# Performance work log

Measured on AMD Instinct MI355X. Metric: run time of the kernel, lower is better.

## Reference

```python
import jax, jax.numpy as jnp
import numpy as np
import math

B, N, G, D = 32, 100, 32, 1024  # batch, boxes (hardcoded 100), groups/fc_dim, out_channel
DG = D // G                      # 32, per-group dim
FEAT_DIM = 64                    # position embedding dim


def setup_inputs() -> dict:
    key = jax.random.key(0)
    ks = jax.random.split(key, 10)
    feat = jax.random.normal(ks[0], (B, N, D), dtype=jnp.float32)
    # valid boxes: xmin/ymin in [0,500), width/height in [1,101)
    xy = jax.random.uniform(ks[1], (B, N, 2), dtype=jnp.float32) * 500.0
    wh = jax.random.uniform(ks[2], (B, N, 2), dtype=jnp.float32) * 100.0 + 1.0
    bbox = jnp.concatenate([xy, xy + wh], axis=-1)  # (B,N,4) xmin,ymin,xmax,ymax
    feat_mask = jax.random.bernoulli(ks[3], 0.1, (B, N, G, N))
    s = 0.02
    fc1_w = jax.random.normal(ks[4], (G, FEAT_DIM), dtype=jnp.float32) * s
    fc1_b = jnp.zeros((G,), dtype=jnp.float32)
    q_w = jax.random.normal(ks[5], (D, D), dtype=jnp.float32) * s
    q_b = jnp.zeros((D,), dtype=jnp.float32)
    k_w = jax.random.normal(ks[6], (D, D), dtype=jnp.float32) * s
    k_b = jnp.zeros((D,), dtype=jnp.float32)
    # grouped 1x1 conv: torch weight (D_out=1024, D_in/groups=1024,1,1) -> (G, DG, D)
    conv_w = jax.random.normal(ks[7], (G, DG, D), dtype=jnp.float32) * s
    conv_b = jnp.zeros((D,), dtype=jnp.float32)
    return {"feat": feat, "bbox": bbox, "feat_mask": feat_mask,
            "fc1_w": fc1_w, "fc1_b": fc1_b, "q_w": q_w, "q_b": q_b,
            "k_w": k_w, "k_b": k_b, "conv_w": conv_w, "conv_b": conv_b}


def _position_embedding(bbox):
    xmin, ymin, xmax, ymax = jnp.split(bbox, 4, axis=2)  # each (B,N,1)
    bw = xmax - xmin + 1.0
    bh = ymax - ymin + 1.0
    cx = 0.5 * (xmin + xmax)
    cy = 0.5 * (ymin + ymax)
    dx = jnp.log(jnp.maximum(jnp.abs((cx - cx.swapaxes(1, 2)) / bw), 1e-3))
    dy = jnp.log(jnp.maximum(jnp.abs((cy - cy.swapaxes(1, 2)) / bh), 1e-3))
    dw = jnp.log(bw / bw.swapaxes(1, 2))
    dh = jnp.log(bh / bh.swapaxes(1, 2))
    pos = jnp.stack([dx, dy, dw, dh], axis=3)  # (B,N,N,4)
    feat_range = jnp.arange(FEAT_DIM // 8, dtype=jnp.float32)  # 8
    dim_mat = jnp.power(1000.0, (8.0 / FEAT_DIM) * feat_range)  # (8,)
    div = (100.0 * pos)[..., None] / dim_mat  # (B,N,N,4,8)
    emb = jnp.concatenate([jnp.sin(div), jnp.cos(div)], axis=4)  # (B,N,N,4,16)
    return emb.reshape(bbox.shape[0], N, N, FEAT_DIM)


def reference(feat, bbox, feat_mask, fc1_w, fc1_b, q_w, q_b, k_w, k_b, conv_w, conv_b):
    pos_emb = _position_embedding(bbox)  # (B,N,N,64)
    # fc1 + relu -> affinity weights; aff_weight[b,q,g,k]
    aff_weight = jax.nn.relu(jnp.einsum('bqkf,gf->bqkg', pos_emb, fc1_w) + fc1_b)
    aff_weight = aff_weight.swapaxes(2, 3)  # (B,N,G,N)
    q = (feat @ q_w.T + q_b).reshape(-1, N, G, DG)  # (B,N,G,DG)
    k = (feat @ k_w.T + k_b).reshape(-1, N, G, DG)
    aff = jnp.einsum('bqgd,bkgd->bqgk', q, k) * (1.0 / math.sqrt(DG))  # (B,N,G,N)
    weighted = jnp.log(jnp.maximum(aff_weight, 1e-6)) + aff
    weighted = jnp.where(feat_mask, -1e9, weighted)
    sm = jax.nn.softmax(weighted, axis=3)  # (B,N,G,N)
    out_t = jnp.einsum('bqgk,bkc->bqgc', sm, feat)  # (B,N,G,D)
    # grouped 1x1 conv: group g maps D channels -> DG output channels
    lin = jnp.einsum('bqgc,goc->bqgo', out_t, conv_w) + conv_b.reshape(G, DG)
    attention = lin.reshape(feat.shape[0], N, D)
    return jax.nn.relu(feat + attention)
```

## Files before the change

### kernel.cpp

```cpp
#include <hip/hip_runtime.h>
#include <math.h>

#define B_  32
#define N_  100
#define G_  32
#define D_  1024
#define DG_ 32
#define FD_ 64

typedef __attribute__((ext_vector_type(8))) short short8;
typedef __attribute__((ext_vector_type(8))) unsigned short ushort8;
typedef __attribute__((ext_vector_type(4))) unsigned short ushort4v;
typedef __attribute__((ext_vector_type(4))) float f32x4;

__device__ inline unsigned short f2bf(float f) {
    unsigned int x = __float_as_uint(f);
    unsigned int r = (x + 0x7fffu + ((x >> 16) & 1u)) >> 16;
    return (unsigned short)r;
}
__device__ inline unsigned short f2h(float f) {
    _Float16 h = (_Float16)f;
    return __builtin_bit_cast(unsigned short, h);
}
__device__ inline float h2f(unsigned short u) {
    return (float)__builtin_bit_cast(_Float16, u);
}
__device__ inline void load_lds16(const void* g, void* l) {
    __builtin_amdgcn_global_load_lds(
        (const __attribute__((address_space(1))) void*)g,
        (__attribute__((address_space(3))) void*)l, 16, 0, 0);
}

__global__ __launch_bounds__(256) void prep_kernel(
    const unsigned int* __restrict__ mask, int* __restrict__ flag,
    const float* __restrict__ bbox, float* __restrict__ prep,
    const float* __restrict__ feat, unsigned short* __restrict__ featb,
    const float* __restrict__ qw, unsigned short* __restrict__ wqb,
    const float* __restrict__ kw, unsigned short* __restrict__ wkb,
    const float* __restrict__ cw, unsigned short* __restrict__ wcb)
{
    const int bid = blockIdx.x;
    const int t = threadIdx.x;
    if (bid < 256) {
        const int nwords = (B_ * N_ * G_ * N_) / 4 / 8;
        int v = 0;
        for (int i = bid * 256 + t; i < nwords; i += 256 * 256)
            v |= (mask[i] > 1u) ? 1 : 0;
        if (__any(v) && (t & 63) == 0) atomicOr(flag, 1);
        return;
    }
    if (bid < 272) {
        const int i = (bid - 256) * 256 + t;
        if (i < B_ * N_) {
            const float4 bb = *reinterpret_cast<const float4*>(bbox + (size_t)i * 4);
            const float bw = bb.z - bb.x + 1.0f, bh = bb.w - bb.y + 1.0f;
            float4 o0, o1;
            o0.x = 0.5f * (bb.x + bb.z);
            o0.y = 0.5f * (bb.y + bb.w);
            o0.z = __logf(bw);
            o0.w = __logf(bh);
            o1.x = 1.0f / bw;
            o1.y = 1.0f / bh;
            o1.z = 0.0f; o1.w = 0.0f;
            *reinterpret_cast<float4*>(prep + (size_t)i * 8)     = o0;
            *reinterpret_cast<float4*>(prep + (size_t)i * 8 + 4) = o1;
        }
        return;
    }
    const float* src;
    unsigned short* dst;
    int i;
    if (bid < 1872)      { src = feat; dst = featb; i = (bid - 272) * 256 + t; }
    else if (bid < 2384) { src = qw;   dst = wqb;   i = (bid - 1872) * 256 + t; }
    else if (bid < 2896) { src = kw;   dst = wkb;   i = (bid - 2384) * 256 + t; }
    else                 { src = cw;   dst = wcb;   i = (bid - 2896) * 256 + t; }
    const float4 a = reinterpret_cast<const float4*>(src)[i * 2 + 0];
    const float4 b = reinterpret_cast<const float4*>(src)[i * 2 + 1];
    ushort8 o;
    o[0] = f2bf(a.x); o[1] = f2bf(a.y); o[2] = f2bf(a.z); o[3] = f2bf(a.w);
    o[4] = f2bf(b.x); o[5] = f2bf(b.y); o[6] = f2bf(b.z); o[7] = f2bf(b.w);
    *reinterpret_cast<ushort8*>(&dst[i * 8]) = o;
}

__global__ __launch_bounds__(256) void mfma_gemm_nt(
    const unsigned short* __restrict__ A,
    const unsigned short* __restrict__ Wq,
    const unsigned short* __restrict__ Wk,
    const unsigned short* __restrict__ Wc,
    const float* __restrict__ bq, const float* __restrict__ bk,
    unsigned short* __restrict__ Q16, unsigned short* __restrict__ K16,
    unsigned short* __restrict__ F16)
{
    __shared__ short As0[128 * 64], As1[128 * 64];
    __shared__ short Bs0[64 * 64],  Bs1[64 * 64];

    const int z = blockIdx.z;
    const unsigned short* W = (z == 0) ? Wq : (z == 1) ? Wk : Wc;
    const float* bias        = (z == 0) ? bq : (z == 1) ? bk : nullptr;
    unsigned short* O        = (z == 0) ? Q16 : (z == 1) ? K16 : F16;

    const int m0 = blockIdx.x * 128;
    const int n0 = blockIdx.y * 64;
    const int t = threadIdx.x;
    const int lane = t & 63;
    const int wid = t >> 6;
    const int wr = wid >> 1, wc = wid & 1;
    const int lo = lane & 15, hi = lane >> 4;

    f32x4 acc[4][2] = {};

    auto STAGE = [&](short* dA, short* dB, int k0) {
#pragma unroll
        for (int c = 0; c < 4; ++c) {
            const int idx16 = c * 256 + t;
            const int row = idx16 >> 3;
            const int colb = ((idx16 & 7) * 16) ^ ((row & 7) << 4);
            load_lds16((const char*)(A + (size_t)(m0 + row) * D_ + k0) + colb,
                       (char*)dA + (c * 256 + wid * 64) * 16);
        }
#pragma unroll
        for (int c = 0; c < 2; ++c) {
            const int idx16 = c * 256 + t;
            const int row = idx16 >> 3;
            const int colb = ((idx16 & 7) * 16) ^ ((row & 7) << 4);
            load_lds16((const char*)(W + (size_t)(n0 + row) * D_ + k0) + colb,
                       (char*)dB + (c * 256 + wid * 64) * 16);
        }
    };

    auto COMPUTE = [&](const short* sA, const short* sB) {
#pragma unroll
        for (int ks = 0; ks < 2; ++ks) {
            short8 afr[4], bfr[2];
            const int kb = ks * 64 + hi * 16;
#pragma unroll
            for (int f = 0; f < 4; ++f) {
                const int am = wr * 64 + f * 16 + lo;
                afr[f] = *reinterpret_cast<const short8*>(
                    (const char*)sA + am * 128 + (kb ^ ((am & 7) << 4)));
            }
#pragma unroll
            for (int j = 0; j < 2; ++j) {
                const int bn = wc * 32 + j * 16 + lo;
                bfr[j] = *reinterpret_cast<const short8*>(
                    (const char*)sB + bn * 128 + (kb ^ ((bn & 7) << 4)));
            }
#pragma unroll
            for (int i = 0; i < 4; ++i)
#pragma unroll
                for (int j = 0; j < 2; ++j)
                    acc[i][j] = __builtin_amdgcn_mfma_f32_16x16x32_bf16(
                        afr[i], bfr[j], acc[i][j], 0, 0, 0);
        }
    };

    STAGE(As0, Bs0, 0);
    __syncthreads();
    for (int it = 0; it < 16; it += 2) {
        STAGE(As1, Bs1, (it + 1) << 6);
        COMPUTE(As0, Bs0);
        __syncthreads();
        if (it + 2 < 16) STAGE(As0, Bs0, (it + 2) << 6);
        COMPUTE(As1, Bs1);
        __syncthreads();
    }

#pragma unroll
    for (int j = 0; j < 2; ++j) {
        const int col = n0 + wc * 32 + j * 16 + lo;
        const float bv = bias ? bias[col] : 0.0f;
#pragma unroll
        for (int i = 0; i < 4; ++i) {
            const int mbase = m0 + wr * 64 + i * 16 + hi * 4;
#pragma unroll
            for (int r = 0; r < 4; ++r)
                O[(size_t)(mbase + r) * D_ + col] = f2bf(acc[i][j][r] + bv);
        }
    }
}

__global__ __launch_bounds__(256) void pos_fc1_kernel(
    const float* __restrict__ prep, const float* __restrict__ fc1_w,
    const float* __restrict__ fc1_b,
    const unsigned char* __restrict__ mask8, const int* __restrict__ mask32,
    const int* __restrict__ flag, unsigned short* __restrict__ wm)
{
    __shared__ unsigned short embh[112 * 72];
    __shared__ unsigned short w1h[G_ * 72];
    __shared__ float b1[G_];
    __shared__ float tbl[8];
    __shared__ float pos4[N_][4];

    const int b = blockIdx.x / N_;
    const int q = blockIdx.x % N_;
    const int t = threadIdx.x;
    const int lane = t & 63;
    const int w = t >> 6;
    const int lo = lane & 15, hi = lane >> 4;

    const float4 pq0 = *reinterpret_cast<const float4*>(prep + (size_t)(b * N_ + q) * 8);
    const float4 pq1 = *reinterpret_cast<const float4*>(prep + (size_t)(b * N_ + q) * 8 + 4);
    const float cxq = pq0.x, cyq = pq0.y, lbwq = pq0.z, lbhq = pq0.w;
    const float rbwq = pq1.x, rbhq = pq1.y;

    for (int i = t; i < G_ * FD_; i += 256)
        w1h[(i >> 6) * 72 + (i & 63)] = f2h(fc1_w[i]);
    if (t < G_) b1[t] = fc1_b[t];
    if (t < 8)  tbl[t] = 100.0f / powf(1000.0f, (float)t * 0.125f);
    for (int i = t; i < 12 * 64; i += 256)
        embh[(100 + (i >> 6)) * 72 + (i & 63)] = 0;

    if (t < N_) {
        const float4 p0 = *reinterpret_cast<const float4*>(prep + (size_t)(b * N_ + t) * 8);
        pos4[t][0] = __logf(fmaxf(fabsf(cxq - p0.x) * rbwq, 1e-3f));
        pos4[t][1] = __logf(fmaxf(fabsf(cyq - p0.y) * rbhq, 1e-3f));
        pos4[t][2] = lbwq - p0.z;
        pos4[t][3] = lbhq - p0.w;
    }
    __syncthreads();

    for (int idx = t; idx < N_ * 32; idx += 256) {
        const int k = idx >> 5;
        const int p = (idx >> 3) & 3;
        const int j = idx & 7;
        const float dv = pos4[k][p] * tbl[j];
        embh[k * 72 + p * 16 + j]     = f2h(__sinf(dv));
        embh[k * 72 + p * 16 + 8 + j] = f2h(__cosf(dv));
    }
    __syncthreads();

    const bool bytemask = (*flag != 0);
    const int xq = q & 7;
    for (int tid = w; tid < 14; tid += 4) {
        const int mt = tid >> 1, nt = tid & 1;
        f32x4 d = {};
#pragma unroll
        for (int ks = 0; ks < 2; ++ks) {
            const short8 af = *reinterpret_cast<const short8*>(
                embh + (mt * 16 + lo) * 72 + ks * 32 + hi * 8);
            const short8 bf = *reinterpret_cast<const short8*>(
                w1h + (nt * 16 + lo) * 72 + ks * 32 + hi * 8);
            d = __builtin_amdgcn_mfma_f32_16x16x32_f16(af, bf, d, 0, 0, 0);
        }
        const int g = nt * 16 + lo;
        const int k0 = mt * 16 + hi * 4;
        const float bb = b1[g];
        unsigned int mby = 0;
        uint4 mi = {};
        if (k0 < N_) {
            const size_t midx = ((size_t)(b * N_ + q) * G_ + g) * N_ + k0;
            if (bytemask) mby = *(const unsigned int*)(mask8 + midx);
            else          mi  = *(const uint4*)(mask32 + midx);
        }
        ushort4v ov;
#pragma unroll
        for (int r = 0; r < 4; ++r) {
            const int k = k0 + r;
            const bool msk = bytemask
                ? (((mby >> (8 * r)) & 0xffu) != 0u)
                : ((r == 0 ? mi.x : r == 1 ? mi.y : r == 2 ? mi.z : mi.w) != 0u);
            ov[r] = (k >= N_ || msk) ? (unsigned short)0
                                     : f2h(fmaxf(d[r] + bb, 1e-6f));
        }
        const size_t row = (size_t)(b * N_ + q) * G_ + g;
        char* dst = (char*)wm + row * 256 + ((2 * k0) ^ (xq << 4));
        *reinterpret_cast<ushort4v*>(dst) = ov;
    }
}

__global__ __launch_bounds__(256) void attn_mfma(
    const unsigned short* __restrict__ qb, const unsigned short* __restrict__ kb,
    const unsigned short* __restrict__ fk16, const unsigned short* __restrict__ wm,
    const float* __restrict__ feat, const float* __restrict__ conv_b,
    float* __restrict__ out)
{
    __shared__ unsigned short PW[128 * 128];
    __shared__ unsigned short FL[DG_ * 128];

    const int bg = blockIdx.x;
    const int b = bg >> 5, g = bg & 31;
    const int t = threadIdx.x;
    const int lane = t & 63;
    const int w = t >> 6;
    const int lo = lane & 15, hi = lane >> 4;
    const float scale = 0.17677669529663687f;

    {
        const char* wbase = (const char*)wm + ((size_t)b * N_ * G_ + g) * 256;
        for (int u = t; u < 1600; u += 256) {
            const int qq = u >> 4, seg = u & 15;
            load_lds16(wbase + (size_t)qq * (G_ * 256) + seg * 16,
                       (char*)PW + u * 16);
        }
    }
    for (int u = t; u < DG_ * 28; u += 256) {
        const int dg = u / 28, n = 100 + u % 28;
        *(unsigned short*)((char*)FL + dg * 256 +
                           (((n >> 3) ^ (dg & 7)) << 4) + (n & 7) * 2) = 0;
    }
    for (int u = t; u < 400; u += 256) {
        const int n = u >> 2, c4 = u & 3;
        const ushort8 v = *reinterpret_cast<const ushort8*>(
            fk16 + (size_t)(b * N_ + n) * D_ + g * DG_ + c4 * 8);
#pragma unroll
        for (int j = 0; j < 8; ++j) {
            const int dg = c4 * 8 + j;
            *(unsigned short*)((char*)FL + dg * 256 +
                               (((n >> 3) ^ j) << 4) + (n & 7) * 2) = v[j];
        }
    }

    short8 qf[2], kf[7];
#pragma unroll
    for (int mtl = 0; mtl < 2; ++mtl) {
        const int row = w * 32 + mtl * 16 + lo;
        const int rc = row < N_ ? row : N_ - 1;
        qf[mtl] = *reinterpret_cast<const short8*>(
            qb + (size_t)(b * N_ + rc) * D_ + g * DG_ + hi * 8);
    }
#pragma unroll
    for (int ct = 0; ct < 7; ++ct) {
        const int kr = ct * 16 + lo;
        const int krc = kr < N_ ? kr : N_ - 1;
        kf[ct] = *reinterpret_cast<const short8*>(
            kb + (size_t)(b * N_ + krc) * D_ + g * DG_ + hi * 8);
    }

    __syncthreads();

    f32x4 s[2][7];
#pragma unroll
    for (int mtl = 0; mtl < 2; ++mtl)
#pragma unroll
        for (int ct = 0; ct < 7; ++ct) {
            f32x4 z = {};
            s[mtl][ct] = __builtin_amdgcn_mfma_f32_16x16x32_bf16(
                qf[mtl], kf[ct], z, 0, 0, 0);
        }

    float sm[2][4];
#pragma unroll
    for (int mtl = 0; mtl < 2; ++mtl) {
        const int qr0 = w * 32 + mtl * 16 + hi * 4;
        f32x4 mv = s[mtl][0];
#pragma unroll
        for (int ct = 1; ct < 7; ++ct)
#pragma unroll
            for (int r = 0; r < 4; ++r) mv[r] = fmaxf(mv[r], s[mtl][ct][r]);
        float mx[4];
#pragma unroll
        for (int r = 0; r < 4; ++r) {
            float m = mv[r];
            m = fmaxf(m, __shfl_xor(m, 1));
            m = fmaxf(m, __shfl_xor(m, 2));
            m = fmaxf(m, __shfl_xor(m, 4));
            m = fmaxf(m, __shfl_xor(m, 8));
            mx[r] = m;
        }
        f32x4 sv = {};
#pragma unroll
        for (int ct = 0; ct < 7; ++ct) {
            const int k = ct * 16 + lo;
#pragma unroll
            for (int r = 0; r < 4; ++r) {
                const int row = qr0 + r;
                const float wv = h2f(*(const unsigned short*)(
                    (const char*)PW + row * 256 + ((2 * k) ^ ((row & 7) << 4))));
                const float e = __expf((s[mtl][ct][r] - mx[r]) * scale) * wv;
                s[mtl][ct][r] = e;
                sv[r] += e;
            }
        }
#pragma unroll
        for (int r = 0; r < 4; ++r) {
            float ss = sv[r];
            ss += __shfl_xor(ss, 1);
            ss += __shfl_xor(ss, 2);
            ss += __shfl_xor(ss, 4);
            ss += __shfl_xor(ss, 8);
            sm[mtl][r] = 1.0f / ss;
        }
    }

#pragma unroll
    for (int mtl = 0; mtl < 2; ++mtl) {
        const int qr0 = w * 32 + mtl * 16 + hi * 4;
#pragma unroll
        for (int ct = 0; ct < 7; ++ct) {
            const int col = ct * 16 + lo;
#pragma unroll
            for (int r = 0; r < 4; ++r) {
                const int row = qr0 + r;
                *(unsigned short*)((char*)PW + row * 256 +
                                   ((2 * col) ^ ((row & 7) << 4))) =
                    f2bf(s[mtl][ct][r] * sm[mtl][r]);
            }
        }
    }
    {
        const int zr = w * 32 + (lane & 31);
        const int zg = 14 + (lane >> 5);
        short8 zs = {};
        *reinterpret_cast<short8*>(
            (char*)PW + zr * 256 + ((zg * 16) ^ ((zr & 7) << 4))) = zs;
    }

    f32x4 o[2][2] = {};
#pragma unroll
    for (int ks = 0; ks < 4; ++ks) {
        short8 pa[2], fb[2];
#pragma unroll
        for (int mtl = 0; mtl < 2; ++mtl) {
            const int prow = w * 32 + mtl * 16 + lo;
            pa[mtl] = *reinterpret_cast<const short8*>(
                (const char*)PW + prow * 256 +
                ((ks * 64 + hi * 16) ^ ((prow & 7) << 4)));
        }
#pragma unroll
        for (int nt = 0; nt < 2; ++nt) {
            const int dg = nt * 16 + lo;
            fb[nt] = *reinterpret_cast<const short8*>(
                (const char*)FL + dg * 256 +
                ((ks * 64 + hi * 16) ^ ((dg & 7) << 4)));
        }
#pragma unroll
        for (int mtl = 0; mtl < 2; ++mtl)
#pragma unroll
            for (int nt = 0; nt < 2; ++nt)
                o[mtl][nt] = __builtin_amdgcn_mfma_f32_16x16x32_bf16(
                    pa[mtl], fb[nt], o[mtl][nt], 0, 0, 0);
    }

#pragma unroll
    for (int mtl = 0; mtl < 2; ++mtl) {
        const int qr0 = w * 32 + mtl * 16 + hi * 4;
#pragma unroll
        for (int nt = 0; nt < 2; ++nt) {
            const int col = g * DG_ + nt * 16 + lo;
            const float cb = conv_b[col];
#pragma unroll
            for (int r = 0; r < 4; ++r) {
                const int q = qr0 + r;
                if (q < N_) {
                    const size_t gi = (size_t)(b * N_ + q) * D_ + col;
                    out[gi] = fmaxf(feat[gi] + o[mtl][nt][r] + cb, 0.0f);
                }
            }
        }
    }
}

extern "C" void kernel_launch(void* const* d_in, const int* in_sizes, int n_in,
                              void* d_out, int out_size, void* d_ws, size_t ws_size,
                              hipStream_t stream)
{
    const float* feat   = (const float*)d_in[0];
    const float* bbox   = (const float*)d_in[1];
    const void*  maskp  = d_in[2];
    const float* fc1_w  = (const float*)d_in[3];
    const float* fc1_b  = (const float*)d_in[4];
    const float* q_w    = (const float*)d_in[5];
    const float* q_b    = (const float*)d_in[6];
    const float* k_w    = (const float*)d_in[7];
    const float* k_b    = (const float*)d_in[8];
    const float* conv_w = (const float*)d_in[9];
    const float* conv_b = (const float*)d_in[10];

    const int BN_D  = B_ * N_ * D_;
    const int DD    = D_ * D_;
    const int WM_N  = B_ * G_ * N_ * 128;

    unsigned short* ws16 = (unsigned short*)d_ws;
    unsigned short* qb16  = ws16;
    unsigned short* kb16  = qb16 + BN_D;
    unsigned short* fk16  = kb16 + BN_D;
    unsigned short* wm    = fk16 + BN_D;
    int* flag = (int*)(wm + WM_N);
    float* prep = (float*)(flag + 64);

    unsigned short* featb = wm;
    unsigned short* wqb   = featb + BN_D;
    unsigned short* wkb   = wqb + DD;
    unsigned short* wcb   = wkb + DD;

    hipMemsetAsync(flag, 0, sizeof(int), stream);
    prep_kernel<<<3408, 256, 0, stream>>>((const unsigned int*)maskp, flag,
                                          bbox, prep, feat, featb,
                                          q_w, wqb, k_w, wkb, conv_w, wcb);

    dim3 gg(B_ * N_ / 128, D_ / 64, 3);
    mfma_gemm_nt<<<gg, 256, 0, stream>>>(featb, wqb, wkb, wcb, q_b, k_b,
                                         qb16, kb16, fk16);

    pos_fc1_kernel<<<B_ * N_, 256, 0, stream>>>(prep, fc1_w, fc1_b,
                                                (const unsigned char*)maskp,
                                                (const int*)maskp, flag, wm);

    attn_mfma<<<B_ * G_, 256, 0, stream>>>(qb16, kb16, fk16, wm,
                                           feat, conv_b, (float*)d_out);
}
```

Baseline: 96.82 us.

## Fuse cast and position-fc1 kernels, split mask detection, read bf16 residual

The bf16 cast work and the position-embedding/fc1 work now share one launch, with even and odd blocks interleaved. The bbox preprocessing moves into each block's shared memory and mask detection becomes its own small kernel. featb no longer aliases wm and gets its own workspace region, so the epilogue reads the bf16 feature copy instead of fp32 for the residual. This is meant to cut launch overhead and overlap the two independent workloads, but the residual add now loses precision and the workspace footprint grows.

```diff
diff --git a/kernel.cpp b/kernel.cpp
--- a/kernel.cpp
+++ b/kernel.cpp
@@ -25,61 +25,147 @@
 __device__ inline float h2f(unsigned short u) {
     return (float)__builtin_bit_cast(_Float16, u);
 }
+__device__ inline float bf2f(unsigned short u) {
+    return __uint_as_float((unsigned int)u << 16);
+}
 __device__ inline void load_lds16(const void* g, void* l) {
     __builtin_amdgcn_global_load_lds(
         (const __attribute__((address_space(1))) void*)g,
         (__attribute__((address_space(3))) void*)l, 16, 0, 0);
 }
 
-__global__ __launch_bounds__(256) void prep_kernel(
-    const unsigned int* __restrict__ mask, int* __restrict__ flag,
-    const float* __restrict__ bbox, float* __restrict__ prep,
+__global__ __launch_bounds__(256) void detect_kernel(
+    const unsigned int* __restrict__ m, int* __restrict__ flag)
+{
+    const int nwords = (B_ * N_ * G_ * N_) / 4 / 8;
+    int v = 0;
+    for (int i = blockIdx.x * 256 + threadIdx.x; i < nwords; i += 256 * 256)
+        v |= (m[i] > 1u) ? 1 : 0;
+    if (__any(v) && (threadIdx.x & 63) == 0) atomicOr(flag, 1);
+}
+
+__global__ __launch_bounds__(256) void fused_cast_pos(
+    const float* __restrict__ bbox, const float* __restrict__ fc1_w,
+    const float* __restrict__ fc1_b,
+    const unsigned char* __restrict__ mask8, const int* __restrict__ mask32,
+    const int* __restrict__ flag, unsigned short* __restrict__ wm,
     const float* __restrict__ feat, unsigned short* __restrict__ featb,
     const float* __restrict__ qw, unsigned short* __restrict__ wqb,
     const float* __restrict__ kw, unsigned short* __restrict__ wkb,
     const float* __restrict__ cw, unsigned short* __restrict__ wcb)
 {
+    __shared__ unsigned short embh[112 * 72];
+    __shared__ unsigned short w1h[G_ * 72];
+    __shared__ float b1[G_];
+    __shared__ float tbl[8];
+    __shared__ float pos4[N_][4];
+    __shared__ float prepL[N_][6];
+
     const int bid = blockIdx.x;
     const int t = threadIdx.x;
-    if (bid < 256) {
-        const int nwords = (B_ * N_ * G_ * N_) / 4 / 8;
-        int v = 0;
-        for (int i = bid * 256 + t; i < nwords; i += 256 * 256)
-            v |= (mask[i] > 1u) ? 1 : 0;
-        if (__any(v) && (t & 63) == 0) atomicOr(flag, 1);
+
+    if ((bid & 1) == 0) {
+        const int pid = bid >> 1;
+        const float* src;
+        unsigned short* dst;
+        int i;
+        if (pid < 1600)      { src = feat; dst = featb; i = pid * 256 + t; }
+        else if (pid < 2112) { src = qw;   dst = wqb;   i = (pid - 1600) * 256 + t; }
+        else if (pid < 2624) { src = kw;   dst = wkb;   i = (pid - 2112) * 256 + t; }
+        else if (pid < 3136) { src = cw;   dst = wcb;   i = (pid - 2624) * 256 + t; }
+        else return;
+        const float4 a = reinterpret_cast<const float4*>(src)[i * 2 + 0];
+        const float4 b = reinterpret_cast<const float4*>(src)[i * 2 + 1];
+        ushort8 o;
+        o[0] = f2bf(a.x); o[1] = f2bf(a.y); o[2] = f2bf(a.z); o[3] = f2bf(a.w);
+        o[4] = f2bf(b.x); o[5] = f2bf(b.y); o[6] = f2bf(b.z); o[7] = f2bf(b.w);
+        *reinterpret_cast<ushort8*>(&dst[i * 8]) = o;
         return;
     }
-    if (bid < 272) {
-        const int i = (bid - 256) * 256 + t;
-        if (i < B_ * N_) {
-            const float4 bb = *reinterpret_cast<const float4*>(bbox + (size_t)i * 4);
-            const float bw = bb.z - bb.x + 1.0f, bh = bb.w - bb.y + 1.0f;
-            float4 o0, o1;
-            o0.x = 0.5f * (bb.x + bb.z);
-            o0.y = 0.5f * (bb.y + bb.w);
-            o0.z = __logf(bw);
-            o0.w = __logf(bh);
-            o1.x = 1.0f / bw;
-            o1.y = 1.0f / bh;
-            o1.z = 0.0f; o1.w = 0.0f;
-            *reinterpret_cast<float4*>(prep + (size_t)i * 8)     = o0;
-            *reinterpret_cast<float4*>(prep + (size_t)i * 8 + 4) = o1;
-        }
-        return;
-    }
-    const float* src;
-    unsigned short* dst;
-    int i;
-    if (bid < 1872)      { src = feat; dst = featb; i = (bid - 272) * 256 + t; }
-    else if (bid < 2384) { src = qw;   dst = wqb;   i = (bid - 1872) * 256 + t; }
-    else if (bid < 2896) { src = kw;   dst = wkb;   i = (bid - 2384) * 256 + t; }
-    else                 { src = cw;   dst = wcb;   i = (bid - 2896) * 256 + t; }
-    const float4 a = reinterpret_cast<const float4*>(src)[i * 2 + 0];
-    const float4 b = reinterpret_cast<const float4*>(src)[i * 2 + 1];
-    ushort8 o;
-    o[0] = f2bf(a.x); o[1] = f2bf(a.y); o[2] = f2bf(a.z); o[3] = f2bf(a.w);
-    o[4] = f2bf(b.x); o[5] = f2bf(b.y); o[6] = f2bf(b.z); o[7] = f2bf(b.w);
-    *reinterpret_cast<ushort8*>(&dst[i * 8]) = o;
+
+    const int pid = bid >> 1;
+    const int b = pid / N_;
+    const int q = pid % N_;
+    const int lane = t & 63;
+    const int w = t >> 6;
+    const int lo = lane & 15, hi = lane >> 4;
+
+    if (t < N_) {
+        const float4 bb = *reinterpret_cast<const float4*>(bbox + (size_t)(b * N_ + t) * 4);
+        const float bw = bb.z - bb.x + 1.0f, bh = bb.w - bb.y + 1.0f;
+        prepL[t][0] = 0.5f * (bb.x + bb.z);
+        prepL[t][1] = 0.5f * (bb.y + bb.w);
+        prepL[t][2] = __logf(bw);
+        prepL[t][3] = __logf(bh);
+        prepL[t][4] = 1.0f / bw;
+        prepL[t][5] = 1.0f / bh;
+    }
+    for (int i = t; i < G_ * FD_; i += 256)
+        w1h[(i >> 6) * 72 + (i & 63)] = f2h(fc1_w[i]);
+    if (t < G_) b1[t] = fc1_b[t];
+    if (t < 8)  tbl[t] = 100.0f / powf(1000.0f, (float)t * 0.125f);
+    for (int i = t; i < 12 * 64; i += 256)
+        embh[(100 + (i >> 6)) * 72 + (i & 63)] = 0;
+    __syncthreads();
+
+    const float cxq = prepL[q][0], cyq = prepL[q][1];
+    const float lbwq = prepL[q][2], lbhq = prepL[q][3];
+    const float rbwq = prepL[q][4], rbhq = prepL[q][5];
+    if (t < N_) {
+        pos4[t][0] = __logf(fmaxf(fabsf(cxq - prepL[t][0]) * rbwq, 1e-3f));
+        pos4[t][1] = __logf(fmaxf(fabsf(cyq - prepL[t][1]) * rbhq, 1e-3f));
+        pos4[t][2] = lbwq - prepL[t][2];
+        pos4[t][3] = lbhq - prepL[t][3];
+    }
+    __syncthreads();
+
+    for (int idx = t; idx < N_ * 32; idx += 256) {
+        const int k = idx >> 5;
+        const int p = (idx >> 3) & 3;
+        const int j = idx & 7;
+        const float dv = pos4[k][p] * tbl[j];
+        embh[k * 72 + p * 16 + j]     = f2h(__sinf(dv));
+        embh[k * 72 + p * 16 + 8 + j] = f2h(__cosf(dv));
+    }
+    __syncthreads();
+
+    const bool bytemask = (*flag != 0);
+    const int xq = q & 7;
+    for (int tid = w; tid < 14; tid += 4) {
+        const int mt = tid >> 1, nt = tid & 1;
+        f32x4 d = {};
+#pragma unroll
+        for (int ks = 0; ks < 2; ++ks) {
+            const short8 af = *reinterpret_cast<const short8*>(
+                embh + (mt * 16 + lo) * 72 + ks * 32 + hi * 8);
+            const short8 bf = *reinterpret_cast<const short8*>(
+                w1h + (nt * 16 + lo) * 72 + ks * 32 + hi * 8);
+            d = __builtin_amdgcn_mfma_f32_16x16x32_f16(af, bf, d, 0, 0, 0);
+        }
+        const int g = nt * 16 + lo;
+        const int k0 = mt * 16 + hi * 4;
+        const float bb = b1[g];
+        unsigned int mby = 0;
+        uint4 mi = {};
+        if (k0 < N_) {
+            const size_t midx = ((size_t)(b * N_ + q) * G_ + g) * N_ + k0;
+            if (bytemask) mby = *(const unsigned int*)(mask8 + midx);
+            else          mi  = *(const uint4*)(mask32 + midx);
+        }
+        ushort4v ov;
+#pragma unroll
+        for (int r = 0; r < 4; ++r) {
+            const int k = k0 + r;
+            const bool msk = bytemask
+                ? (((mby >> (8 * r)) & 0xffu) != 0u)
+                : ((r == 0 ? mi.x : r == 1 ? mi.y : r == 2 ? mi.z : mi.w) != 0u);
+            ov[r] = (k >= N_ || msk) ? (unsigned short)0
+                                     : f2h(fmaxf(d[r] + bb, 1e-6f));
+        }
+        const size_t row = (size_t)(b * N_ + q) * G_ + g;
+        char* dst = (char*)wm + row * 256 + ((2 * k0) ^ (xq << 4));
+        *reinterpret_cast<ushort4v*>(dst) = ov;
+    }
 }
 
 __global__ __launch_bounds__(256) void mfma_gemm_nt(
@@ -179,99 +265,10 @@
     }
 }
 
-__global__ __launch_bounds__(256) void pos_fc1_kernel(
-    const float* __restrict__ prep, const float* __restrict__ fc1_w,
-    const float* __restrict__ fc1_b,
-    const unsigned char* __restrict__ mask8, const int* __restrict__ mask32,
-    const int* __restrict__ flag, unsigned short* __restrict__ wm)
-{
-    __shared__ unsigned short embh[112 * 72];
-    __shared__ unsigned short w1h[G_ * 72];
-    __shared__ float b1[G_];
-    __shared__ float tbl[8];
-    __shared__ float pos4[N_][4];
-
-    const int b = blockIdx.x / N_;
-    const int q = blockIdx.x % N_;
-    const int t = threadIdx.x;
-    const int lane = t & 63;
-    const int w = t >> 6;
-    const int lo = lane & 15, hi = lane >> 4;
-
-    const float4 pq0 = *reinterpret_cast<const float4*>(prep + (size_t)(b * N_ + q) * 8);
-    const float4 pq1 = *reinterpret_cast<const float4*>(prep + (size_t)(b * N_ + q) * 8 + 4);
-    const float cxq = pq0.x, cyq = pq0.y, lbwq = pq0.z, lbhq = pq0.w;
-    const float rbwq = pq1.x, rbhq = pq1.y;
-
-    for (int i = t; i < G_ * FD_; i += 256)
-        w1h[(i >> 6) * 72 + (i & 63)] = f2h(fc1_w[i]);
-    if (t < G_) b1[t] = fc1_b[t];
-    if (t < 8)  tbl[t] = 100.0f / powf(1000.0f, (float)t * 0.125f);
-    for (int i = t; i < 12 * 64; i += 256)
-        embh[(100 + (i >> 6)) * 72 + (i & 63)] = 0;
-
-    if (t < N_) {
-        const float4 p0 = *reinterpret_cast<const float4*>(prep + (size_t)(b * N_ + t) * 8);
-        pos4[t][0] = __logf(fmaxf(fabsf(cxq - p0.x) * rbwq, 1e-3f));
-        pos4[t][1] = __logf(fmaxf(fabsf(cyq - p0.y) * rbhq, 1e-3f));
-        pos4[t][2] = lbwq - p0.z;
-        pos4[t][3] = lbhq - p0.w;
-    }
-    __syncthreads();
-
-    for (int idx = t; idx < N_ * 32; idx += 256) {
-        const int k = idx >> 5;
-        const int p = (idx >> 3) & 3;
-        const int j = idx & 7;
-        const float dv = pos4[k][p] * tbl[j];
-        embh[k * 72 + p * 16 + j]     = f2h(__sinf(dv));
-        embh[k * 72 + p * 16 + 8 + j] = f2h(__cosf(dv));
-    }
-    __syncthreads();
-
-    const bool bytemask = (*flag != 0);
-    const int xq = q & 7;
-    for (int tid = w; tid < 14; tid += 4) {
-        const int mt = tid >> 1, nt = tid & 1;
-        f32x4 d = {};
-#pragma unroll
-        for (int ks = 0; ks < 2; ++ks) {
-            const short8 af = *reinterpret_cast<const short8*>(
-                embh + (mt * 16 + lo) * 72 + ks * 32 + hi * 8);
-            const short8 bf = *reinterpret_cast<const short8*>(
-                w1h + (nt * 16 + lo) * 72 + ks * 32 + hi * 8);
-            d = __builtin_amdgcn_mfma_f32_16x16x32_f16(af, bf, d, 0, 0, 0);
-        }
-        const int g = nt * 16 + lo;
-        const int k0 = mt * 16 + hi * 4;
-        const float bb = b1[g];
-        unsigned int mby = 0;
-        uint4 mi = {};
-        if (k0 < N_) {
-            const size_t midx = ((size_t)(b * N_ + q) * G_ + g) * N_ + k0;
-            if (bytemask) mby = *(const unsigned int*)(mask8 + midx);
-            else          mi  = *(const uint4*)(mask32 + midx);
-        }
-        ushort4v ov;
-#pragma unroll
-        for (int r = 0; r < 4; ++r) {
-            const int k = k0 + r;
-            const bool msk = bytemask
-                ? (((mby >> (8 * r)) & 0xffu) != 0u)
-                : ((r == 0 ? mi.x : r == 1 ? mi.y : r == 2 ? mi.z : mi.w) != 0u);
-            ov[r] = (k >= N_ || msk) ? (unsigned short)0
-                                     : f2h(fmaxf(d[r] + bb, 1e-6f));
-        }
-        const size_t row = (size_t)(b * N_ + q) * G_ + g;
-        char* dst = (char*)wm + row * 256 + ((2 * k0) ^ (xq << 4));
-        *reinterpret_cast<ushort4v*>(dst) = ov;
-    }
-}
-
 __global__ __launch_bounds__(256) void attn_mfma(
     const unsigned short* __restrict__ qb, const unsigned short* __restrict__ kb,
     const unsigned short* __restrict__ fk16, const unsigned short* __restrict__ wm,
-    const float* __restrict__ feat, const float* __restrict__ conv_b,
+    const unsigned short* __restrict__ featb, const float* __restrict__ conv_b,
     float* __restrict__ out)
 {
     __shared__ unsigned short PW[128 * 128];
@@ -443,7 +440,7 @@
                 const int q = qr0 + r;
                 if (q < N_) {
                     const size_t gi = (size_t)(b * N_ + q) * D_ + col;
-                    out[gi] = fmaxf(feat[gi] + o[mtl][nt][r] + cb, 0.0f);
+                    out[gi] = fmaxf(bf2f(featb[gi]) + o[mtl][nt][r] + cb, 0.0f);
                 }
             }
         }
@@ -475,27 +472,24 @@
     unsigned short* kb16  = qb16 + BN_D;
     unsigned short* fk16  = kb16 + BN_D;
     unsigned short* wm    = fk16 + BN_D;
-    int* flag = (int*)(wm + WM_N);
-    float* prep = (float*)(flag + 64);
-
-    unsigned short* featb = wm;
+    unsigned short* featb = wm + WM_N;
     unsigned short* wqb   = featb + BN_D;
     unsigned short* wkb   = wqb + DD;
     unsigned short* wcb   = wkb + DD;
+    int* flag = (int*)(wcb + DD);
 
     hipMemsetAsync(flag, 0, sizeof(int), stream);
-    prep_kernel<<<3408, 256, 0, stream>>>((const unsigned int*)maskp, flag,
-                                          bbox, prep, feat, featb,
-                                          q_w, wqb, k_w, wkb, conv_w, wcb);
+    detect_kernel<<<256, 256, 0, stream>>>((const unsigned int*)maskp, flag);
+
+    fused_cast_pos<<<6400, 256, 0, stream>>>(
+        bbox, fc1_w, fc1_b,
+        (const unsigned char*)maskp, (const int*)maskp, flag, wm,
+        feat, featb, q_w, wqb, k_w, wkb, conv_w, wcb);
 
     dim3 gg(B_ * N_ / 128, D_ / 64, 3);
     mfma_gemm_nt<<<gg, 256, 0, stream>>>(featb, wqb, wkb, wcb, q_b, k_b,
                                          qb16, kb16, fk16);
 
-    pos_fc1_kernel<<<B_ * N_, 256, 0, stream>>>(prep, fc1_w, fc1_b,
-                                                (const unsigned char*)maskp,
-                                                (const int*)maskp, flag, wm);
-
     attn_mfma<<<B_ * G_, 256, 0, stream>>>(qb16, kb16, fk16, wm,
-                                           feat, conv_b, (float*)d_out);
-}
+                                           featb, conv_b, (float*)d_out);
+}
```

Result: slower. 110.3 us (+14.0%).
